# Kernel optimization log

Hardware: AMD Instinct MI355X
Metric: run time of the kernel (lower is better)

Reference implementation:

```python
import jax, jax.numpy as jnp
import numpy as np

B, S, N, C = 8, 256, 256, 64
NH = 8
H, W = 256, 256
D = N * C // NH  # per-head channel dim = 2048
EPS = 1e-12


def window_reverse(windows, ws, Hh, Ww, Cc):
    # windows: (B, S, N, C) -> (B, H*W, C)
    b = windows.shape[0]
    x = windows.reshape(b, Hh // ws[0], Ww // ws[1], ws[0], ws[1], Cc)
    x = x.transpose(0, 1, 3, 2, 4, 5).reshape(b, Hh, Ww, Cc).reshape(b, Hh * Ww, Cc)
    return x


def window_partition(x, ws):
    # x: (B, H, W, C) -> (B, nWin, winElems, C)
    b, hh, ww, cc = x.shape
    x = x.reshape(b, hh // ws[0], ws[0], ww // ws[1], ws[1], cc)
    return x.transpose(0, 1, 3, 2, 4, 5).reshape(b, (hh // ws[0]) * (ww // ws[1]), ws[0] * ws[1], cc)


def setup_inputs() -> dict:
    key = jax.random.key(0)
    ks = jax.random.split(key, 6)
    x = jax.random.normal(ks[0], (B, S, N, C), dtype=jnp.float32)
    qkv_w = jax.random.normal(ks[1], (4 * C, C), dtype=jnp.float32) * 0.02
    qkv_b = jnp.zeros((4 * C,), dtype=jnp.float32)
    proj_w = jax.random.normal(ks[2], (C, C), dtype=jnp.float32) * 0.02
    proj_b = jnp.zeros((C,), dtype=jnp.float32)
    temperature1 = jnp.ones((NH, 1, 1), dtype=jnp.float32)
    temperature2 = jnp.ones((NH, 1, 1), dtype=jnp.float32)
    return {"x": x, "qkv_w": qkv_w, "qkv_b": qkv_b, "proj_w": proj_w,
            "proj_b": proj_b, "temperature1": temperature1, "temperature2": temperature2}


def reference(x, qkv_w, qkv_b, proj_w, proj_b, temperature1, temperature2):
    b, s, n, c = x.shape
    xf = x.reshape(b, s * n, c)
    # fused 4-way qkv projection (q, k, v_H, v_V)
    qkvv = (xf @ qkv_w.T + qkv_b).reshape(b, s, 4, NH, D).transpose(2, 0, 3, 1, 4)
    q, k, v_H, v_V = qkvv[0], qkvv[1], qkvv[2], qkvv[3]  # each (B, NH, S, D)

    # reorient v_V from H-windows (columns) to V-windows (rows)
    v_V = v_V.transpose(0, 2, 1, 3).reshape(b, s, n, c)       # (B,S,N,C)
    v_V = v_V.transpose(0, 2, 1, 3)                           # (B,N,S,C)
    v_V = window_reverse(v_V, (H, 1), H, W, c).reshape(b, H, W, c)
    v_V = window_partition(v_V, (1, W))                       # (B,H,W,C)
    v_V = v_V.transpose(0, 2, 1, 3)                           # (B,W,H,C) == (B,S,N,C)
    v_V = v_V.reshape(b, s, NH, D).transpose(0, 2, 1, 3)      # (B,NH,S,D)

    # cosine attention over S with per-head temperature
    qn = q / jnp.maximum(jnp.linalg.norm(q, axis=-1, keepdims=True), EPS)
    kn = k / jnp.maximum(jnp.linalg.norm(k, axis=-1, keepdims=True), EPS)
    sim = jnp.einsum('bhsd,bhtd->bhst', qn, kn)  # (B,NH,S,S)
    attn_H = jax.nn.softmax(sim * temperature1, axis=-1)
    attn_V = jax.nn.softmax(sim * temperature2, axis=-1)

    x_H = jnp.einsum('bhst,bhtd->bhsd', attn_H, v_H).transpose(0, 2, 1, 3).reshape(b, s * n, c)
    x_V = jnp.einsum('bhst,bhtd->bhsd', attn_V, v_V).transpose(0, 2, 1, 3).reshape(b, s * n, c)

    out = (x_H + x_V) @ proj_w.T + proj_b
    return out.reshape(b, s, n, c)
```

## Files before the change

kernel.cpp:

```cpp
#include <hip/hip_runtime.h>


using half_t = _Float16;
using half8 = __attribute__((ext_vector_type(8))) _Float16;
using f32x4 = __attribute__((ext_vector_type(4))) float;

#define NTOK 524288

#define WS_Q      0
#define WS_K      67108864
#define WS_VH     134217728
#define WS_VV     201326592
#define WS_XHV    268435456
#define WS_NQ     335544320
#define WS_NK     335609856
#define WS_WH     335675392
#define WS_WP     335708160

__global__ void kW0(const float* __restrict__ qkv_w, const float* __restrict__ proj_w,
                    half_t* __restrict__ Wh, half_t* __restrict__ Wp) {
    int tid = threadIdx.x;
    for (int i = tid; i < 256 * 64; i += 256) Wh[i] = (half_t)qkv_w[i];
    for (int i = tid; i < 64 * 64; i += 256) Wp[i] = (half_t)proj_w[i];
}

__device__ inline void y_tile_mfma(const float* __restrict__ xb,
                                   const half_t* __restrict__ Wh,
                                   int tbase, int hi, int lo,
                                   f32x4 (&acc)[4][4], int wave, int lane) {
    const int l15 = lane & 15, quad = lane >> 4;
#pragma unroll
    for (int kc = 0; kc < 2; ++kc) {
        const int c = kc * 32 + quad * 8;
        half8 afr[4];
#pragma unroll
        for (int mt = 0; mt < 4; ++mt) {
            int m = mt * 16 + l15;
            int token = tbase + (m >> 3) * hi + (m & 7) * lo;
            const float* p = xb + (size_t)token * 64 + c;
            f32x4 f0 = *(const f32x4*)p;
            f32x4 f1 = *(const f32x4*)(p + 4);
            half8 a;
            a[0] = (half_t)f0[0]; a[1] = (half_t)f0[1]; a[2] = (half_t)f0[2]; a[3] = (half_t)f0[3];
            a[4] = (half_t)f1[0]; a[5] = (half_t)f1[1]; a[6] = (half_t)f1[2]; a[7] = (half_t)f1[3];
            afr[mt] = a;
        }
#pragma unroll
        for (int i = 0; i < 4; ++i) {
            int j = (wave * 4 + i) * 16 + l15;
            half8 bfr = *(const half8*)(Wh + j * 64 + c);
#pragma unroll
            for (int mt = 0; mt < 4; ++mt)
                acc[mt][i] = __builtin_amdgcn_mfma_f32_16x16x32_f16(afr[mt], bfr, acc[mt][i], 0, 0, 0);
        }
    }
}

__device__ inline void y_dump_rowmajor(f32x4 (&acc)[4][4], const float* __restrict__ qkv_b,
                                       half_t* ylds, int wave, int lane) {
    const int l15 = lane & 15, quad = lane >> 4;
#pragma unroll
    for (int i = 0; i < 4; ++i) {
        int j = (wave * 4 + i) * 16 + l15;
        float bj = qkv_b[j];
#pragma unroll
        for (int mt = 0; mt < 4; ++mt)
#pragma unroll
            for (int r = 0; r < 4; ++r)
                ylds[(mt * 16 + quad * 4 + r) * 264 + j] = (half_t)(acc[mt][i][r] + bj);
    }
}

__device__ inline void y_dump_transposed(f32x4 (&acc)[4][4], const float* __restrict__ qkv_b,
                                         half_t* yldsT, int wave, int lane) {
    const int l15 = lane & 15, quad = lane >> 4;
#pragma unroll
    for (int i = 0; i < 4; ++i) {
        int j = (wave * 4 + i) * 16 + l15;
        float bj = qkv_b[j];
#pragma unroll
        for (int mt = 0; mt < 4; ++mt)
#pragma unroll
            for (int r = 0; r < 4; ++r)
                yldsT[j * 72 + mt * 16 + quad * 4 + r] = (half_t)(acc[mt][i][r] + bj);
    }
}

__global__ __launch_bounds__(256) void kA1(const float* __restrict__ x,
                                           const half_t* __restrict__ Wh,
                                           const float* __restrict__ qkv_b,
                                           half_t* __restrict__ Q, half_t* __restrict__ K,
                                           float* __restrict__ normQ, float* __restrict__ normK) {
    __shared__ half_t ylds[64 * 264];
    __shared__ float scr[256];
    int idx = blockIdx.x;
    int sb = idx & 31; idx >>= 5;
    int h = idx & 7; idx >>= 3;
    int g = idx & 1; int b = idx >> 1;
    int s0 = sb * 8;
    int n0 = g * 64 + h * 8;
    int tid = threadIdx.x, wave = tid >> 6, lane = tid & 63;
    const float* xb = x + (size_t)b * 65536 * 64;
    f32x4 acc[4][4];
#pragma unroll
    for (int a = 0; a < 4; ++a)
#pragma unroll
        for (int c = 0; c < 4; ++c) acc[a][c] = {0.f, 0.f, 0.f, 0.f};
    y_tile_mfma(xb, Wh, s0 * 256 + n0, 256, 1, acc, wave, lane);
    y_dump_rowmajor(acc, qkv_b, ylds, wave, lane);
    __syncthreads();
    half_t* dst = (g == 0 ? Q : K) + ((size_t)(b * 8 + h) * 256 + s0) * 2048;
    int ns = tid >> 5, jc = (tid & 31) * 8;
#pragma unroll
    for (int si = 0; si < 8; ++si) {
        half8 v = *(const half8*)&ylds[(si * 8 + ns) * 264 + jc];
        *(half8*)(dst + (size_t)si * 2048 + ns * 256 + jc) = v;
    }
    float sum = 0.f;
#pragma unroll
    for (int nn = 0; nn < 8; ++nn) {
        half8 v = *(const half8*)&ylds[((tid >> 5) * 8 + nn) * 264 + (tid & 31) * 8];
#pragma unroll
        for (int e = 0; e < 8; ++e) { float f = (float)v[e]; sum += f * f; }
    }
    scr[tid] = sum;
    __syncthreads();
    if (tid < 8) {
        float s = 0.f;
        for (int k2 = 0; k2 < 32; ++k2) s += scr[tid * 32 + k2];
        float* nd = (g == 0 ? normQ : normK);
        nd[(b * 8 + h) * 256 + s0 + tid] = s;
    }
}

__global__ __launch_bounds__(256) void kA2H(const float* __restrict__ x,
                                            const half_t* __restrict__ Wh,
                                            const float* __restrict__ qkv_b,
                                            half_t* __restrict__ VH) {
    __shared__ half_t yldsT[256 * 72];
    int idx = blockIdx.x;
    int sb = idx & 3; idx >>= 2;
    int nn = idx & 63; int b = idx >> 6;
    int h = nn >> 3, ns = nn & 7;
    int n = 128 + nn;
    int s0 = sb * 64;
    int tid = threadIdx.x, wave = tid >> 6, lane = tid & 63;
    const float* xb = x + (size_t)b * 65536 * 64;
    f32x4 acc[4][4];
#pragma unroll
    for (int a = 0; a < 4; ++a)
#pragma unroll
        for (int c = 0; c < 4; ++c) acc[a][c] = {0.f, 0.f, 0.f, 0.f};
    y_tile_mfma(xb, Wh, s0 * 256 + n, 2048, 256, acc, wave, lane);
    y_dump_transposed(acc, qkv_b, yldsT, wave, lane);
    __syncthreads();
    int jl = lane >> 3, tc = lane & 7;
    half_t* base = VH + ((size_t)(b * 8 + h) * 2048 + ns * 256) * 256 + s0 + tc * 8;
#pragma unroll
    for (int u = 0; u < 8; ++u) {
        int j = wave * 64 + u * 8 + jl;
        half8 v = *(const half8*)&yldsT[j * 72 + tc * 8];
        *(half8*)(base + (size_t)j * 256) = v;
    }
}

__global__ __launch_bounds__(256) void kA2V(const float* __restrict__ x,
                                            const half_t* __restrict__ Wh,
                                            const float* __restrict__ qkv_b,
                                            half_t* __restrict__ VV) {
    __shared__ half_t yldsT[256 * 72];
    int idx = blockIdx.x;
    int st = idx & 255; int b = idx >> 8;
    int h = st >> 5;
    int tid = threadIdx.x, wave = tid >> 6, lane = tid & 63;
    const float* xb = x + (size_t)b * 65536 * 64;
    f32x4 acc[4][4];
#pragma unroll
    for (int a = 0; a < 4; ++a)
#pragma unroll
        for (int c = 0; c < 4; ++c) acc[a][c] = {0.f, 0.f, 0.f, 0.f};
    y_tile_mfma(xb, Wh, st * 256 + 192, 8, 1, acc, wave, lane);
    y_dump_transposed(acc, qkv_b, yldsT, wave, lane);
    __syncthreads();
    int dl = lane >> 3, tc = lane & 7;
    int mbase = wave * 16 + (tc >> 2) * 8 + (tc & 3) * 2;
    half_t* base = VV + ((size_t)(b * 8 + h) * 2048 + (st & 31) * 64) * 256 + wave * 64 + tc * 8;
#pragma unroll
    for (int u = 0; u < 8; ++u) {
        int dm = u * 8 + dl;
        half8 v;
#pragma unroll
        for (int e = 0; e < 8; ++e)
            v[e] = yldsT[((e & 3) * 64 + dm) * 72 + mbase + (e >> 2)];
        *(half8*)(base + (size_t)dm * 256) = v;
    }
}

__global__ __launch_bounds__(1024, 4) void kB(const half_t* __restrict__ Q, const half_t* __restrict__ K,
                                              const half_t* __restrict__ VH, const half_t* __restrict__ VV,
                                              const float* __restrict__ normQ, const float* __restrict__ normK,
                                              const float* __restrict__ temp1, const float* __restrict__ temp2,
                                              half_t* __restrict__ xhv) {
    extern __shared__ char smem[];
    half_t* PH = (half_t*)smem;
    half_t* PV = (half_t*)(smem + 33792);
    float* redA = (float*)(smem + 67584);
    float* redB = (float*)(smem + 71680);
    float* mH  = (float*)(smem + 75776);
    float* mV  = (float*)(smem + 76032);
    float* rHs = (float*)(smem + 76288);
    float* rVs = (float*)(smem + 76544);
    float* rq  = (float*)(smem + 76800);
    float* rk  = (float*)(smem + 77056);

    int idx = blockIdx.x;
    int bh = idx & 63;
    int sqb = idx >> 6;
    int h = bh & 7, b = bh >> 3;
    int sq0 = sqb * 64;
    int tid = threadIdx.x, wave = tid >> 6, lane = tid & 63;
    int l15 = lane & 15, quad = lane >> 4;
    float t1 = temp1[h], t2 = temp2[h];
    const half_t* Qb = Q + (size_t)bh * 256 * 2048;
    const half_t* Kb = K + (size_t)bh * 256 * 2048;
    const half_t* VHb = VH + (size_t)bh * 2048 * 256;
    const half_t* VVb = VV + (size_t)bh * 2048 * 256;

    if (tid < 64) rq[tid] = 1.f / fmaxf(sqrtf(normQ[bh * 256 + sq0 + tid]), 1e-12f);
    if (tid < 256) rk[tid] = 1.f / fmaxf(sqrtf(normK[bh * 256 + tid]), 1e-12f);
    __syncthreads();

    {
        f32x4 acc1[4];
#pragma unroll
        for (int a = 0; a < 4; ++a) acc1[a] = {0.f, 0.f, 0.f, 0.f};
        const int tcol = wave * 16 + l15;
        for (int kc = 0; kc < 64; ++kc) {
            int d = kc * 32 + quad * 8;
            half8 bfr = *(const half8*)(Kb + (size_t)tcol * 2048 + d);
#pragma unroll
            for (int mt = 0; mt < 4; ++mt) {
                half8 afr = *(const half8*)(Qb + (size_t)(sq0 + mt * 16 + l15) * 2048 + d);
                acc1[mt] = __builtin_amdgcn_mfma_f32_16x16x32_f16(afr, bfr, acc1[mt], 0, 0, 0);
            }
        }
        float rkt = rk[tcol];
#pragma unroll
        for (int mt = 0; mt < 4; ++mt)
#pragma unroll
            for (int r = 0; r < 4; ++r) {
                int row = mt * 16 + quad * 4 + r;
                PH[row * 264 + tcol] = (half_t)(acc1[mt][r] * rq[row] * rkt);
            }
    }
    __syncthreads();

    int r_ = tid & 63, c16 = tid >> 6;
    half_t* phrow = &PH[r_ * 264 + c16 * 16];
    half_t* pvrow = &PV[r_ * 264 + c16 * 16];
    float mx = -3.4e38f, mn = 3.4e38f;
#pragma unroll
    for (int i2 = 0; i2 < 16; ++i2) { float v = (float)phrow[i2]; mx = fmaxf(mx, v); mn = fminf(mn, v); }
    redA[tid] = mx; redB[tid] = mn;
    __syncthreads();
    if (tid < 64) {
        float amx = -3.4e38f, amn = 3.4e38f;
#pragma unroll
        for (int q2 = 0; q2 < 16; ++q2) {
            amx = fmaxf(amx, redA[q2 * 64 + tid]);
            amn = fminf(amn, redB[q2 * 64 + tid]);
        }
        mH[tid] = (t1 >= 0.f) ? t1 * amx : t1 * amn;
        mV[tid] = (t2 >= 0.f) ? t2 * amx : t2 * amn;
    }
    __syncthreads();
    float mh = mH[r_], mv = mV[r_];
    float sh = 0.f, sv = 0.f;
#pragma unroll
    for (int i2 = 0; i2 < 16; ++i2) {
        float v = (float)phrow[i2];
        sh += __expf(v * t1 - mh);
        sv += __expf(v * t2 - mv);
    }
    redA[tid] = sh; redB[tid] = sv;
    __syncthreads();
    if (tid < 64) {
        float ash = 0.f, asv = 0.f;
#pragma unroll
        for (int q2 = 0; q2 < 16; ++q2) { ash += redA[q2 * 64 + tid]; asv += redB[q2 * 64 + tid]; }
        rHs[tid] = 1.f / ash;
        rVs[tid] = 1.f / asv;
    }
    __syncthreads();
    float rh = rHs[r_], rv = rVs[r_];
#pragma unroll
    for (int i2 = 0; i2 < 16; ++i2) {
        float v = (float)phrow[i2];
        phrow[i2] = (half_t)(__expf(v * t1 - mh) * rh);
        pvrow[i2] = (half_t)(__expf(v * t2 - mv) * rv);
    }
    __syncthreads();

#pragma unroll
    for (int i2 = 0; i2 < 2; ++i2) {
        int d0 = wave * 64 + i2 * 1024;
        f32x4 acc2[4][4];
#pragma unroll
        for (int a = 0; a < 4; ++a)
#pragma unroll
            for (int c = 0; c < 4; ++c) acc2[a][c] = {0.f, 0.f, 0.f, 0.f};
        for (int kc = 0; kc < 8; ++kc) {
            int tk = kc * 32 + quad * 8;
            half8 afr[4];
#pragma unroll
            for (int mt = 0; mt < 4; ++mt)
                afr[mt] = *(const half8*)&PH[(mt * 16 + l15) * 264 + tk];
#pragma unroll
            for (int nt = 0; nt < 4; ++nt) {
                half8 bfr = *(const half8*)(VHb + (size_t)(d0 + nt * 16 + l15) * 256 + tk);
#pragma unroll
                for (int mt = 0; mt < 4; ++mt)
                    acc2[mt][nt] = __builtin_amdgcn_mfma_f32_16x16x32_f16(afr[mt], bfr, acc2[mt][nt], 0, 0, 0);
            }
#pragma unroll
            for (int mt = 0; mt < 4; ++mt)
                afr[mt] = *(const half8*)&PV[(mt * 16 + l15) * 264 + tk];
#pragma unroll
            for (int nt = 0; nt < 4; ++nt) {
                half8 bfr = *(const half8*)(VVb + (size_t)(d0 + nt * 16 + l15) * 256 + tk);
#pragma unroll
                for (int mt = 0; mt < 4; ++mt)
                    acc2[mt][nt] = __builtin_amdgcn_mfma_f32_16x16x32_f16(afr[mt], bfr, acc2[mt][nt], 0, 0, 0);
            }
        }
        int db = wave + i2 * 16;
#pragma unroll
        for (int mt = 0; mt < 4; ++mt)
#pragma unroll
            for (int nt = 0; nt < 4; ++nt) {
                int c = nt * 16 + l15;
#pragma unroll
                for (int r = 0; r < 4; ++r) {
                    int srow = mt * 16 + quad * 4 + r;
                    size_t tk_idx = (size_t)b * 65536 + (size_t)(sq0 + srow) * 256 + h * 32 + db;
                    xhv[tk_idx * 64 + c] = (half_t)acc2[mt][nt][r];
                }
            }
    }
}

__global__ __launch_bounds__(256) void kC(const half_t* __restrict__ xhv, const half_t* __restrict__ Wp,
                                          const float* __restrict__ proj_b, float* __restrict__ out) {
    __shared__ float ot[64 * 68];
    int tid = threadIdx.x, wave = tid >> 6, lane = tid & 63;
    int l15 = lane & 15, quad = lane >> 4;
    size_t T0 = (size_t)blockIdx.x * 64;
    f32x4 acc[4];
#pragma unroll
    for (int a = 0; a < 4; ++a) acc[a] = {0.f, 0.f, 0.f, 0.f};
#pragma unroll
    for (int kc = 0; kc < 2; ++kc) {
        int c = kc * 32 + quad * 8;
        half8 bfr = *(const half8*)(Wp + (wave * 16 + l15) * 64 + c);
#pragma unroll
        for (int mt = 0; mt < 4; ++mt) {
            half8 afr = *(const half8*)(xhv + (T0 + mt * 16 + l15) * 64 + c);
            acc[mt] = __builtin_amdgcn_mfma_f32_16x16x32_f16(afr, bfr, acc[mt], 0, 0, 0);
        }
    }
    float bj = proj_b[wave * 16 + l15];
#pragma unroll
    for (int mt = 0; mt < 4; ++mt)
#pragma unroll
        for (int r = 0; r < 4; ++r)
            ot[(mt * 16 + quad * 4 + r) * 68 + wave * 16 + l15] = acc[mt][r] + bj;
    __syncthreads();
    int row = tid >> 2;
#pragma unroll
    for (int u = 0; u < 4; ++u) {
        int col = (tid & 3) * 4 + u * 16;
        f32x4 v = *(const f32x4*)&ot[row * 68 + col];
        *(f32x4*)(out + (T0 + row) * 64 + col) = v;
    }
}

extern "C" void kernel_launch(void* const* d_in, const int* in_sizes, int n_in,
                              void* d_out, int out_size, void* d_ws, size_t ws_size,
                              hipStream_t stream) {
    const float* x      = (const float*)d_in[0];
    const float* qkv_w  = (const float*)d_in[1];
    const float* qkv_b  = (const float*)d_in[2];
    const float* proj_w = (const float*)d_in[3];
    const float* proj_b = (const float*)d_in[4];
    const float* temp1  = (const float*)d_in[5];
    const float* temp2  = (const float*)d_in[6];
    char* ws = (char*)d_ws;
    half_t* Q   = (half_t*)(ws + WS_Q);
    half_t* K   = (half_t*)(ws + WS_K);
    half_t* VH  = (half_t*)(ws + WS_VH);
    half_t* VV  = (half_t*)(ws + WS_VV);
    half_t* xhv = (half_t*)(ws + WS_XHV);
    float* normQ = (float*)(ws + WS_NQ);
    float* normK = (float*)(ws + WS_NK);
    half_t* Wh  = (half_t*)(ws + WS_WH);
    half_t* Wp  = (half_t*)(ws + WS_WP);
    float* out = (float*)d_out;

    hipFuncSetAttribute((const void*)kB, hipFuncAttributeMaxDynamicSharedMemorySize, 78080);

    kW0<<<1, 256, 0, stream>>>(qkv_w, proj_w, Wh, Wp);
    kA1<<<4096, 256, 0, stream>>>(x, Wh, qkv_b, Q, K, normQ, normK);
    kA2H<<<2048, 256, 0, stream>>>(x, Wh, qkv_b, VH);
    kA2V<<<2048, 256, 0, stream>>>(x, Wh, qkv_b, VV);
    kB<<<256, 1024, 78080, stream>>>(Q, K, VH, VV, normQ, normK, temp1, temp2, xhv);
    kC<<<8192, 256, 0, stream>>>(xhv, Wp, proj_b, out);
}
```

Measured before the change: 664.4 us.

## Stage Q/K tiles into LDS with async double-buffered loads in QK^T

```diff
diff --git a/kernel.cpp b/kernel.cpp
--- a/kernel.cpp
+++ b/kernel.cpp
@@ -6,6 +6,10 @@
 using f32x4 = __attribute__((ext_vector_type(4))) float;
 
 #define NTOK 524288
+
+#define GLDS(g, l) __builtin_amdgcn_global_load_lds( \
+    (const __attribute__((address_space(1))) void*)(g), \
+    (__attribute__((address_space(3))) void*)(l), 16, 0, 0)
 
 #define WS_Q      0
 #define WS_K      67108864
@@ -202,16 +206,20 @@
                                               const float* __restrict__ temp1, const float* __restrict__ temp2,
                                               half_t* __restrict__ xhv) {
     extern __shared__ char smem[];
-    half_t* PH = (half_t*)smem;
-    half_t* PV = (half_t*)(smem + 33792);
-    float* redA = (float*)(smem + 67584);
-    float* redB = (float*)(smem + 71680);
-    float* mH  = (float*)(smem + 75776);
-    float* mV  = (float*)(smem + 76032);
-    float* rHs = (float*)(smem + 76288);
-    float* rVs = (float*)(smem + 76544);
-    float* rq  = (float*)(smem + 76800);
-    float* rk  = (float*)(smem + 77056);
+    char* Ks0 = smem;
+    char* Ks1 = smem + 32768;
+    char* Qs0 = smem + 65536;
+    char* Qs1 = smem + 73728;
+    half_t* PH = (half_t*)(smem + 81920);
+    half_t* PV = (half_t*)(smem + 115712);
+    float* redA = (float*)(smem + 149504);
+    float* redB = (float*)(smem + 153600);
+    float* mH  = (float*)(smem + 157696);
+    float* mV  = (float*)(smem + 157952);
+    float* rHs = (float*)(smem + 158208);
+    float* rVs = (float*)(smem + 158464);
+    float* rq  = (float*)(smem + 158720);
+    float* rk  = (float*)(smem + 158976);
 
     int idx = blockIdx.x;
     int bh = idx & 63;
@@ -228,21 +236,52 @@
 
     if (tid < 64) rq[tid] = 1.f / fmaxf(sqrtf(normQ[bh * 256 + sq0 + tid]), 1e-12f);
     if (tid < 256) rk[tid] = 1.f / fmaxf(sqrtf(normK[bh * 256 + tid]), 1e-12f);
-    __syncthreads();
 
     {
+        const int l7 = lane & 7, l8 = lane >> 3;
+        const int swzh = (l7 ^ (l8 & 7)) * 8;
+        const half_t* gK0 = Kb + (size_t)(wave * 8 + l8) * 2048 + swzh;
+        const half_t* gK1 = Kb + (size_t)(128 + wave * 8 + l8) * 2048 + swzh;
+        const half_t* gQ  = Qb + (size_t)(sq0 + (wave & 7) * 8 + l8) * 2048 + swzh;
+
+        auto STAGE = [&](int kk, char* KsB, char* QsB) {
+            const int off = kk * 64;
+            GLDS(gK0 + off, KsB + wave * 1024);
+            GLDS(gK1 + off, KsB + 16384 + wave * 1024);
+            if (wave < 8) GLDS(gQ + off, QsB + wave * 1024);
+        };
+
         f32x4 acc1[4];
 #pragma unroll
         for (int a = 0; a < 4; ++a) acc1[a] = {0.f, 0.f, 0.f, 0.f};
         const int tcol = wave * 16 + l15;
-        for (int kc = 0; kc < 64; ++kc) {
-            int d = kc * 32 + quad * 8;
-            half8 bfr = *(const half8*)(Kb + (size_t)tcol * 2048 + d);
-#pragma unroll
-            for (int mt = 0; mt < 4; ++mt) {
-                half8 afr = *(const half8*)(Qb + (size_t)(sq0 + mt * 16 + l15) * 2048 + d);
-                acc1[mt] = __builtin_amdgcn_mfma_f32_16x16x32_f16(afr, bfr, acc1[mt], 0, 0, 0);
+        const int ts7 = tcol & 7;
+
+        auto COMPUTE = [&](const char* KsB_, const char* QsB_) {
+            const half_t* KsB = (const half_t*)KsB_;
+            const half_t* QsB = (const half_t*)QsB_;
+#pragma unroll
+            for (int sub = 0; sub < 2; ++sub) {
+                int c16 = sub * 4 + quad;
+                half8 bfr = *(const half8*)(KsB + tcol * 64 + (c16 ^ ts7) * 8);
+#pragma unroll
+                for (int mt = 0; mt < 4; ++mt) {
+                    int m = mt * 16 + l15;
+                    half8 afr = *(const half8*)(QsB + m * 64 + (c16 ^ (m & 7)) * 8);
+                    acc1[mt] = __builtin_amdgcn_mfma_f32_16x16x32_f16(afr, bfr, acc1[mt], 0, 0, 0);
+                }
             }
+        };
+
+        STAGE(0, Ks0, Qs0);
+        __syncthreads();
+        for (int kk = 0; kk < 32; kk += 2) {
+            if (kk + 1 < 32) STAGE(kk + 1, Ks1, Qs1);
+            COMPUTE(Ks0, Qs0);
+            __syncthreads();
+            if (kk + 2 < 32) STAGE(kk + 2, Ks0, Qs0);
+            COMPUTE(Ks1, Qs1);
+            __syncthreads();
         }
         float rkt = rk[tcol];
 #pragma unroll
@@ -255,9 +294,9 @@
     }
     __syncthreads();
 
-    int r_ = tid & 63, c16 = tid >> 6;
-    half_t* phrow = &PH[r_ * 264 + c16 * 16];
-    half_t* pvrow = &PV[r_ * 264 + c16 * 16];
+    int r_ = tid & 63, cc = tid >> 6;
+    half_t* phrow = &PH[r_ * 264 + cc * 16];
+    half_t* pvrow = &PV[r_ * 264 + cc * 16];
     float mx = -3.4e38f, mn = 3.4e38f;
 #pragma unroll
     for (int i2 = 0; i2 < 16; ++i2) { float v = (float)phrow[i2]; mx = fmaxf(mx, v); mn = fminf(mn, v); }
@@ -406,12 +445,12 @@
     half_t* Wp  = (half_t*)(ws + WS_WP);
     float* out = (float*)d_out;
 
-    hipFuncSetAttribute((const void*)kB, hipFuncAttributeMaxDynamicSharedMemorySize, 78080);
+    hipFuncSetAttribute((const void*)kB, hipFuncAttributeMaxDynamicSharedMemorySize, 160000);
 
     kW0<<<1, 256, 0, stream>>>(qkv_w, proj_w, Wh, Wp);
     kA1<<<4096, 256, 0, stream>>>(x, Wh, qkv_b, Q, K, normQ, normK);
     kA2H<<<2048, 256, 0, stream>>>(x, Wh, qkv_b, VH);
     kA2V<<<2048, 256, 0, stream>>>(x, Wh, qkv_b, VV);
-    kB<<<256, 1024, 78080, stream>>>(Q, K, VH, VV, normQ, normK, temp1, temp2, xhv);
+    kB<<<256, 1024, 160000, stream>>>(Q, K, VH, VV, normQ, normK, temp1, temp2, xhv);
     kC<<<8192, 256, 0, stream>>>(xhv, Wp, proj_b, out);
 }
```

After: 605.9 us. 8.8% less time.
